# Kernel tuning notes

Hardware: AMD Instinct MI355X
Metric: run time of the kernel (lower is better)

Reference implementation:

```python
import jax, jax.numpy as jnp
import numpy as np

B, L, D, H, DFF, C = 16, 1024, 256, 4, 2048, 3
NS, NC = 4, 4
DH = D // H


def _ln(x, g, b):
    m = x.mean(-1, keepdims=True)
    v = ((x - m) ** 2).mean(-1, keepdims=True)
    return (x - m) / jnp.sqrt(v + 1e-5) * g + b


def setup_inputs() -> dict:
    key = jax.random.key(0)
    ks = jax.random.split(key, 24)
    n = lambda k, s: jax.random.normal(k, s, jnp.float32) * 0.02
    return {
        'shape_idxs': jax.random.randint(ks[0], (B, L), 0, NS, jnp.int32),
        'color_idxs': jax.random.randint(ks[1], (B, L), 0, NC, jnp.int32),
        'shape_emb': n(ks[2], (NS, D)),
        'color_emb': n(ks[3], (NC, D)),
        'Wq': n(ks[4], (D, D)), 'bq': jnp.zeros((D,)),
        'Wk': n(ks[5], (D, D)), 'bk': jnp.zeros((D,)),
        'Wv': n(ks[6], (D, D)), 'bv': jnp.zeros((D,)),
        'Wo': n(ks[7], (D, D)), 'bo': jnp.zeros((D,)),
        'g1': jnp.ones((D,)), 'be1': jnp.zeros((D,)),
        'W1': n(ks[8], (D, DFF)), 'bf1': jnp.zeros((DFF,)),
        'W2': n(ks[9], (DFF, D)), 'bf2': jnp.zeros((D,)),
        'g2': jnp.ones((D,)), 'be2': jnp.zeros((D,)),
        'Wl': n(ks[10], (D, C)), 'bl': jnp.zeros((C,)),
        'Wp1': n(ks[11], (D, D)), 'bp1': jnp.zeros((D,)),
        'Wp2': n(ks[12], (D, 1)), 'bp2': jnp.zeros((1,)),
        'wc': n(ks[13], (1, 1)), 'bc': jnp.zeros((1,)),
    }


def reference(shape_idxs, color_idxs, shape_emb, color_emb, Wq, bq, Wk, bk, Wv, bv,
              Wo, bo, g1, be1, W1, bf1, W2, bf2, g2, be2, Wl, bl,
              Wp1, bp1, Wp2, bp2, wc, bc):
    # embed (dropout is identity in eval)
    x = shape_emb[shape_idxs] + color_emb[color_idxs]  # [B,L,D]
    # post-norm transformer encoder layer (PyTorch default)
    heads = lambda t: t.reshape(B, L, H, DH)
    q, k, v = heads(x @ Wq + bq), heads(x @ Wk + bk), heads(x @ Wv + bv)
    scores = jnp.einsum('blhd,bmhd->bhlm', q, k) / jnp.sqrt(jnp.float32(DH))
    attn = jax.nn.softmax(scores, axis=-1)
    ctx = jnp.einsum('bhlm,bmhd->blhd', attn, v).reshape(B, L, D)
    y = _ln(x + ctx @ Wo + bo, g1, be1)
    ff = jax.nn.relu(y @ W1 + bf1) @ W2 + bf2
    y = _ln(y + ff, g2, be2)  # trans_out [B,L,D]
    # latent logits / KL(prior || probs) with batchmean reduction
    logits = y @ Wl + bl
    logp = jax.nn.log_softmax(logits, axis=-1)
    prior = 1.0 / C
    kl_loss = jnp.sum(prior * (jnp.log(jnp.float32(prior)) - logp)) / B
    # data-dependent boundary segmentation (argmax of probs == argmax of logits)
    boundaries = (jnp.argmax(logits, axis=-1) == 0)
    boundaries = boundaries.at[:, 0].set(True)
    closed = boundaries & (jnp.arange(L) > 0)  # closure at l>0 ends segment at l
    seg_id = jnp.cumsum(closed.astype(jnp.int32), axis=1) - closed  # exclusive cumsum
    gid = (jnp.arange(B)[:, None] * L + seg_id).reshape(-1)  # global segment ids
    sums = jax.ops.segment_sum(y.reshape(B * L, D), gid, num_segments=B * L)
    counts = jax.ops.segment_sum(jnp.ones((B * L,), jnp.float32), gid, num_segments=B * L)
    means = sums / jnp.maximum(counts, 1.0)[:, None]  # per-segment mean [B*L,D]
    # predicate net + composition, mean over valid segments
    preds = jax.nn.sigmoid(jax.nn.relu(means @ Wp1 + bp1) @ Wp2 + bp2)  # [B*L,1]
    comp = (preds * wc[0, 0] + bc[0]).reshape(B, L)
    valid = (counts > 0).reshape(B, L).astype(jnp.float32)
    mean_comp = jnp.sum(comp * valid, axis=1) / jnp.sum(valid, axis=1)
    final_scores = jax.nn.sigmoid(mean_comp)
    return final_scores, kl_loss
```

## Files before the change

### kernel.cpp

```cpp
#include <hip/hip_runtime.h>


typedef unsigned short u16;
typedef u16    u16x4  __attribute__((ext_vector_type(4)));
typedef u16    u16x8  __attribute__((ext_vector_type(8)));
typedef __bf16 bf16x8 __attribute__((ext_vector_type(8)));
typedef float  f32x4  __attribute__((ext_vector_type(4)));

__device__ __forceinline__ float bf2f(u16 u) {
    union { unsigned int i; float f; } v; v.i = ((unsigned int)u) << 16; return v.f;
}
__device__ __forceinline__ u16 f2bf(float f) {
    union { float f; unsigned int i; } v; v.f = f;
    unsigned int r = (v.i + 0x7FFFu + ((v.i >> 16) & 1u)) >> 16;
    return (u16)r;
}
__device__ __forceinline__ u16 f2bf_fast(float f) {
    union { __bf16 h; u16 u; } v; v.h = (__bf16)f; return v.u;
}
__device__ __forceinline__ void gll16(const u16* g, u16* l) {
    __builtin_amdgcn_global_load_lds((__attribute__((address_space(1))) void*)(u16*)g,
                                     (__attribute__((address_space(3))) void*)l, 16, 0, 0);
}

__global__ void k_dzero(int* __restrict__ diag, float* __restrict__ acc) {
    int t = threadIdx.x;
    if (t < 16) diag[t] = 0;
    if (t < 33) acc[t] = 0.f;
}
__global__ __launch_bounds__(256) void k_detect(const u16* __restrict__ w1raw,
                                                int* __restrict__ diag) {
    int i = blockIdx.x * 256 + threadIdx.x;
    int bad = 0;
    for (int k = i; k < 65536; k += 64 * 256) {
        unsigned v = w1raw[k] & 0x7FFFu;
        if (v >= 0x7F80u) bad++;
    }
    for (int off = 32; off >= 1; off >>= 1) bad += __shfl_xor(bad, off);
    __shared__ int bs[4];
    if ((threadIdx.x & 63) == 0) bs[threadIdx.x >> 6] = bad;
    __syncthreads();
    if (threadIdx.x == 0) {
        int tot = bs[0] + bs[1] + bs[2] + bs[3];
        if (tot) atomicAdd(&diag[14], tot);
        __threadfence();
        int ticket = atomicAdd(&diag[13], 1);
        if (ticket == 63) {
            int cnt = atomicAdd(&diag[14], 0);
            diag[15] = (cnt > 16) ? 1 : 0;
        }
    }
}

struct IngestTab {
    const void* src[26];
    unsigned    dstoff[26];
    int         n[26];
    float       scale[26];
};
__global__ __launch_bounds__(256) void k_ingest(IngestTab tab, u16* __restrict__ ing,
                                                const int* __restrict__ diag) {
    int t = blockIdx.y;
    int n = tab.n[t];
    int m = diag[15];
    float sc = tab.scale[t];
    u16* dst = ing + tab.dstoff[t];
    for (int i = blockIdx.x * 256 + threadIdx.x; i < n; i += gridDim.x * 256) {
        float v = m ? ((const float*)tab.src[t])[i] : bf2f(((const u16*)tab.src[t])[i]);
        dst[i] = f2bf(v * sc);
    }
}
__global__ void k_sentinel_f32(float* __restrict__ out, int code) {
    int t = threadIdx.x;
    if (t < 17) out[t] = (float)code;
}

struct TransTab {
    const u16* src[7];
    u16*       dst[7];
    int        K[7], N[7];
    int        tstart[8];
};
__global__ __launch_bounds__(256) void k_trans_all(TransTab tt) {
    __shared__ u16 tile[32][33];
    int bx = blockIdx.x;
    int wgt = 0;
#pragma unroll
    for (int i = 1; i < 7; ++i) if (bx >= tt.tstart[i]) wgt = i;
    int local = bx - tt.tstart[wgt];
    int K = tt.K[wgt], N = tt.N[wgt];
    int ntx = N >> 5;
    int txt = local % ntx, tyt = local / ntx;
    const u16* W = tt.src[wgt];
    u16* Wt = tt.dst[wgt];
    int tx = threadIdx.x & 31, ty = threadIdx.x >> 5;
    int n = txt * 32 + tx;
    for (int i = ty; i < 32; i += 8) {
        int k = tyt * 32 + i;
        tile[i][tx] = W[(size_t)k * N + n];
    }
    __syncthreads();
    int k2 = tyt * 32 + tx;
    for (int i = ty; i < 32; i += 8) {
        int n2 = txt * 32 + i;
        Wt[(size_t)n2 * K + k2] = tile[tx][i];
    }
}

__global__ __launch_bounds__(256) void k_embed(const int* __restrict__ si,
                                               const int* __restrict__ ci,
                                               const u16* __restrict__ se,
                                               const u16* __restrict__ ce,
                                               u16* __restrict__ X) {
    int t = blockIdx.x * 256 + threadIdx.x;
    int row = t >> 5, seg = (t & 31) * 8;
    int s = si[row], c = ci[row];
    u16x8 a = *(const u16x8*)&se[s * 256 + seg];
    u16x8 b = *(const u16x8*)&ce[c * 256 + seg];
    u16x8 o;
#pragma unroll
    for (int e = 0; e < 8; ++e) o[e] = f2bf(bf2f(a[e]) + bf2f(b[e]));
    *(u16x8*)&X[(size_t)row * 256 + seg] = o;
}

__global__ __launch_bounds__(256) void k_gemm_bt(const u16* __restrict__ A,
                                                 const u16* __restrict__ Bt,
                                                 const u16* __restrict__ bias,
                                                 u16* __restrict__ C,
                                                 int N, int K, int relu, int gx) {
    __shared__ u16 As[128][32];
    __shared__ u16 Bs[128][32];
    const int tid = threadIdx.x;
    const int xcd = blockIdx.x & 7, j = blockIdx.x >> 3;
    const int m0 = (xcd * 16 + j / gx) * 128, n0 = (j % gx) * 128;
    const int lane = tid & 63, wid = tid >> 6;
    const int wm = (wid & 1) * 64, wn = (wid >> 1) * 64;
    const int m16 = lane & 15, quad = lane >> 4;
    f32x4 acc[4][4] = {};
    const int arow = tid >> 2;
    const int ac8  = (tid & 3) * 8;
    const u16* Ap0 = A  + (size_t)(m0 + arow) * K + ac8;
    const u16* Ap1 = A  + (size_t)(m0 + 64 + arow) * K + ac8;
    const u16* Bp0 = Bt + (size_t)(n0 + arow) * K + ac8;
    const u16* Bp1 = Bt + (size_t)(n0 + 64 + arow) * K + ac8;
    u16* lA0 = &As[arow][ac8];
    u16* lA1 = &As[64 + arow][ac8];
    u16* lB0 = &Bs[arow][ac8];
    u16* lB1 = &Bs[64 + arow][ac8];

    for (int k0 = 0; k0 < K; k0 += 32) {
        __syncthreads();
        gll16(Ap0 + k0, lA0);
        gll16(Ap1 + k0, lA1);
        gll16(Bp0 + k0, lB0);
        gll16(Bp1 + k0, lB1);
        __syncthreads();
        bf16x8 af[4], bfv[4];
#pragma unroll
        for (int i = 0; i < 4; ++i)
            af[i] = *(const bf16x8*)&As[wm + i * 16 + m16][quad * 8];
#pragma unroll
        for (int j2 = 0; j2 < 4; ++j2)
            bfv[j2] = *(const bf16x8*)&Bs[wn + j2 * 16 + m16][quad * 8];
#pragma unroll
        for (int i = 0; i < 4; ++i)
#pragma unroll
            for (int j2 = 0; j2 < 4; ++j2)
                acc[i][j2] = __builtin_amdgcn_mfma_f32_16x16x32_bf16(
                    af[i], bfv[j2], acc[i][j2], 0, 0, 0);
    }

#pragma unroll
    for (int i = 0; i < 4; ++i) {
        int row = m0 + wm + i * 16 + quad * 4;
#pragma unroll
        for (int j2 = 0; j2 < 4; ++j2) {
            int col = n0 + wn + j2 * 16 + m16;
            float bv = bf2f(bias[col]);
#pragma unroll
            for (int r = 0; r < 4; ++r) {
                float v = acc[i][j2][r] + bv;
                if (relu) v = fmaxf(v, 0.f);
                C[(size_t)(row + r) * N + col] = f2bf_fast(v);
            }
        }
    }
}

__global__ __launch_bounds__(256) void k_gemm64(const u16* __restrict__ A,
                                                const u16* __restrict__ Bt,
                                                const u16* __restrict__ bias,
                                                u16* __restrict__ C,
                                                int N, int K, int relu,
                                                int gx, int mtpx,
                                                const float* __restrict__ gate,
                                                u16* __restrict__ vt) {
    __shared__ u16 As0[64][32], As1[64][32];
    __shared__ u16 Bs0[128][32], Bs1[128][32];
    const int tid = threadIdx.x;
    const int xcd = blockIdx.x & 7, j = blockIdx.x >> 3;
    const int m0 = (xcd * mtpx + j / gx) * 64, n0 = (j % gx) * 128;
    if (gate && gate[m0] == 0.f) return;
    const int vmode = (vt != nullptr) && (n0 >= 512);
    const int lane = tid & 63, wid = tid >> 6;
    const int wm = (wid & 1) * 32, wn = (wid >> 1) * 64;
    const int m16 = lane & 15, quad = lane >> 4;
    f32x4 acc[2][4] = {};
    const int arow = tid >> 2;
    const int ac8  = (tid & 3) * 8;
    const u16* Ap  = A  + (size_t)(m0 + arow) * K + ac8;
    const u16* Bp0 = Bt + (size_t)(n0 + arow) * K + ac8;
    const u16* Bp1 = Bt + (size_t)(n0 + 64 + arow) * K + ac8;
    u16* lA0  = &As0[arow][ac8];
    u16* lA1  = &As1[arow][ac8];
    u16* lB00 = &Bs0[arow][ac8];
    u16* lB01 = &Bs0[64 + arow][ac8];
    u16* lB10 = &Bs1[arow][ac8];
    u16* lB11 = &Bs1[64 + arow][ac8];

    for (int k0 = 0; k0 < K; k0 += 64) {
        __syncthreads();
        gll16(Ap + k0,        lA0);
        gll16(Ap + k0 + 32,   lA1);
        gll16(Bp0 + k0,       lB00);
        gll16(Bp0 + k0 + 32,  lB10);
        gll16(Bp1 + k0,       lB01);
        gll16(Bp1 + k0 + 32,  lB11);
        __syncthreads();
#pragma unroll
        for (int ks = 0; ks < 2; ++ks) {
            bf16x8 af[2], bfv[4];
#pragma unroll
            for (int i = 0; i < 2; ++i)
                af[i] = ks == 0 ? *(const bf16x8*)&As0[wm + i * 16 + m16][quad * 8]
                                : *(const bf16x8*)&As1[wm + i * 16 + m16][quad * 8];
#pragma unroll
            for (int j2 = 0; j2 < 4; ++j2)
                bfv[j2] = ks == 0 ? *(const bf16x8*)&Bs0[wn + j2 * 16 + m16][quad * 8]
                                  : *(const bf16x8*)&Bs1[wn + j2 * 16 + m16][quad * 8];
#pragma unroll
            for (int i = 0; i < 2; ++i)
#pragma unroll
                for (int j2 = 0; j2 < 4; ++j2)
                    acc[i][j2] = __builtin_amdgcn_mfma_f32_16x16x32_bf16(
                        af[i], bfv[j2], acc[i][j2], 0, 0, 0);
        }
    }

#pragma unroll
    for (int i = 0; i < 2; ++i) {
        int row = m0 + wm + i * 16 + quad * 4;
#pragma unroll
        for (int j2 = 0; j2 < 4; ++j2) {
            int col = n0 + wn + j2 * 16 + m16;
            float bv = bf2f(bias[col]);
            if (vmode) {
                int ch = col - 512;
                u16x4 o;
#pragma unroll
                for (int r = 0; r < 4; ++r) o[r] = f2bf_fast(acc[i][j2][r] + bv);
                size_t vb = ((size_t)((row >> 10) * 4 + (ch >> 6)) * 64 + (ch & 63)) * 1024
                          + (row & 1023);
                *(u16x4*)&vt[vb] = o;
            } else {
#pragma unroll
                for (int r = 0; r < 4; ++r) {
                    float v = acc[i][j2][r] + bv;
                    if (relu) v = fmaxf(v, 0.f);
                    C[(size_t)(row + r) * N + col] = f2bf_fast(v);
                }
            }
        }
    }
}

__global__ __launch_bounds__(256) void k_attn_mfma(const u16* __restrict__ QKV,
                                                   const u16* __restrict__ VT,
                                                   u16* __restrict__ CTX) {
    __shared__ u16 Ks[64][72];
    __shared__ u16 Vts[64][72];
    __shared__ u16 Ps[4][16][72];
    const int tid = threadIdx.x, lane = tid & 63, w = tid >> 6;
    const int quad = lane >> 4, c = lane & 15;
    const int blk = blockIdx.x;
    const int xcd = blk & 7, local = blk >> 3;
    const int bh = xcd * 8 + (local >> 4);
    const int qt = local & 15;
    const int b = bh >> 2, h = bh & 3;
    const int qrow0 = b * 1024 + qt * 64;

    const u16* qptr = QKV + (size_t)(qrow0 + w * 16 + c) * 768 + h * 64;
    bf16x8 aq0 = *(const bf16x8*)(qptr + quad * 8);
    bf16x8 aq1 = *(const bf16x8*)(qptr + 32 + quad * 8);

    f32x4 acc_o[4] = {};
    float l_part[4] = {0.f, 0.f, 0.f, 0.f};

    const u16* kbase  = QKV + (size_t)(b * 1024) * 768 + 256 + h * 64;
    const u16* vtbase = VT + (size_t)(bh * 64) * 1024;
    const int skk = tid >> 3, sc8 = (tid & 7) * 8;

    for (int t = 0; t < 16; ++t) {
        __syncthreads();
#pragma unroll
        for (int it = 0; it < 2; ++it) {
            int rr = skk + 32 * it;
            *(u16x8*)&Ks[rr][sc8]  = *(const u16x8*)(kbase + (size_t)(t * 64 + rr) * 768 + sc8);
            *(u16x8*)&Vts[rr][sc8] = *(const u16x8*)(vtbase + (size_t)rr * 1024 + t * 64 + sc8);
        }
        __syncthreads();

        f32x4 s[4];
#pragma unroll
        for (int nt = 0; nt < 4; ++nt) {
            f32x4 z = {};
            bf16x8 bk0 = *(const bf16x8*)&Ks[nt * 16 + c][quad * 8];
            bf16x8 bk1 = *(const bf16x8*)&Ks[nt * 16 + c][32 + quad * 8];
            z = __builtin_amdgcn_mfma_f32_16x16x32_bf16(aq0, bk0, z, 0, 0, 0);
            s[nt] = __builtin_amdgcn_mfma_f32_16x16x32_bf16(aq1, bk1, z, 0, 0, 0);
        }

#pragma unroll
        for (int nt = 0; nt < 4; ++nt)
#pragma unroll
            for (int r = 0; r < 4; ++r) {
                float pv = exp2f(fminf(s[nt][r], 80.f));
                l_part[r] += pv;
                Ps[w][quad * 4 + r][nt * 16 + c] = f2bf_fast(pv);
            }

#pragma unroll
        for (int ks = 0; ks < 2; ++ks) {
            bf16x8 ap = *(const bf16x8*)&Ps[w][c][ks * 32 + quad * 8];
#pragma unroll
            for (int nt = 0; nt < 4; ++nt) {
                bf16x8 bv = *(const bf16x8*)&Vts[nt * 16 + c][ks * 32 + quad * 8];
                acc_o[nt] = __builtin_amdgcn_mfma_f32_16x16x32_bf16(ap, bv, acc_o[nt], 0, 0, 0);
            }
        }
    }

#pragma unroll
    for (int r = 0; r < 4; ++r) {
#pragma unroll
        for (int off = 1; off <= 8; off <<= 1) l_part[r] += __shfl_xor(l_part[r], off);
    }
#pragma unroll
    for (int nt = 0; nt < 4; ++nt) {
        int col = h * 64 + nt * 16 + c;
#pragma unroll
        for (int r = 0; r < 4; ++r) {
            int row = qrow0 + w * 16 + quad * 4 + r;
            CTX[(size_t)row * 256 + col] = f2bf_fast(acc_o[nt][r] / l_part[r]);
        }
    }
}

__global__ __launch_bounds__(256) void k_ln(const u16* __restrict__ A,
                                            const u16* __restrict__ R,
                                            const u16* __restrict__ g,
                                            const u16* __restrict__ be,
                                            u16* __restrict__ out) {
    int w = threadIdx.x >> 6, lane = threadIdx.x & 63;
    int row = blockIdx.x * 4 + w;
    size_t base = (size_t)row * 256 + lane * 4;
    u16x4 a4 = *(const u16x4*)&A[base];
    u16x4 r4 = *(const u16x4*)&R[base];
    float v[4];
    float s = 0.f, sq = 0.f;
#pragma unroll
    for (int j = 0; j < 4; ++j) {
        v[j] = bf2f(a4[j]) + bf2f(r4[j]);
        s += v[j]; sq += v[j] * v[j];
    }
    for (int off = 32; off >= 1; off >>= 1) { s += __shfl_xor(s, off); sq += __shfl_xor(sq, off); }
    float mean = s * (1.f / 256.f);
    float var  = sq * (1.f / 256.f) - mean * mean;
    float rs   = rsqrtf(var + 1e-5f);
    u16x4 o;
#pragma unroll
    for (int j = 0; j < 4; ++j) {
        int d = lane * 4 + j;
        o[j] = f2bf((v[j] - mean) * rs * bf2f(g[d]) + bf2f(be[d]));
    }
    *(u16x4*)&out[base] = o;
}

__global__ __launch_bounds__(256) void k_logits(const u16* __restrict__ FFO,
                                                const u16* __restrict__ Y1,
                                                const u16* __restrict__ g2,
                                                const u16* __restrict__ be2,
                                                const u16* __restrict__ Wl,
                                                const u16* __restrict__ bl,
                                                u16* __restrict__ Y2,
                                                float* __restrict__ klpart,
                                                int* __restrict__ flags) {
    const int tid = threadIdx.x, lane = tid & 63, w = tid >> 6;
    float wv[4][3], gv[4], bev[4];
#pragma unroll
    for (int j = 0; j < 4; ++j) {
        int d = lane * 4 + j;
        gv[j]  = bf2f(g2[d]);
        bev[j] = bf2f(be2[d]);
#pragma unroll
        for (int c = 0; c < 3; ++c) wv[j][c] = bf2f(Wl[d * 3 + c]);
    }
    const float b0 = bf2f(bl[0]), b1 = bf2f(bl[1]), b2 = bf2f(bl[2]);
    float klsum = 0.f;
    const int row0 = blockIdx.x * 16 + w * 4;
    for (int i = 0; i < 4; ++i) {
        int row = row0 + i;
        size_t base = (size_t)row * 256 + lane * 4;
        u16x4 f4 = *(const u16x4*)&FFO[base];
        u16x4 y4 = *(const u16x4*)&Y1[base];
        float v[4];
        float s = 0.f, sq = 0.f;
#pragma unroll
        for (int j = 0; j < 4; ++j) {
            v[j] = bf2f(f4[j]) + bf2f(y4[j]);
            s += v[j]; sq += v[j] * v[j];
        }
        for (int off = 32; off >= 1; off >>= 1) { s += __shfl_xor(s, off); sq += __shfl_xor(sq, off); }
        float mean = s * (1.f / 256.f);
        float var  = sq * (1.f / 256.f) - mean * mean;
        float rs   = rsqrtf(var + 1e-5f);
        u16x4 o;
        float a0 = 0.f, a1 = 0.f, a2 = 0.f;
#pragma unroll
        for (int j = 0; j < 4; ++j) {
            float yn = (v[j] - mean) * rs * gv[j] + bev[j];
            o[j] = f2bf(yn);
            float y = bf2f(o[j]);
            a0 += y * wv[j][0]; a1 += y * wv[j][1]; a2 += y * wv[j][2];
        }
        *(u16x4*)&Y2[base] = o;
        for (int off = 32; off >= 1; off >>= 1) {
            a0 += __shfl_xor(a0, off); a1 += __shfl_xor(a1, off); a2 += __shfl_xor(a2, off);
        }
        if (lane == 0) {
            float l0 = a0 + b0, l1 = a1 + b1, l2 = a2 + b2;
            float mx = fmaxf(l0, fmaxf(l1, l2));
            float lse = mx + __logf(__expf(l0 - mx) + __expf(l1 - mx) + __expf(l2 - mx));
            klsum += lse - (l0 + l1 + l2) * (1.f / 3.f) - 1.0986122886681098f;
            int am = 0; float bv = l0;
            if (l1 > bv) { bv = l1; am = 1; }
            if (l2 > bv) { am = 2; }
            int l = row & 1023;
            flags[row] = (am == 0 && l != 0) ? 1 : 0;
        }
    }
    __shared__ float kls[4];
    if (lane == 0) kls[w] = klsum;
    __syncthreads();
    if (tid == 0) klpart[blockIdx.x] = kls[0] + kls[1] + kls[2] + kls[3];
}

__global__ void k_scan(const int* __restrict__ flags, int* __restrict__ seg) {
    __shared__ int wsum[16];
    int b = blockIdx.x, t = threadIdx.x;
    int lane = t & 63, w = t >> 6;
    int f = flags[b * 1024 + t];
    int x = f;
#pragma unroll
    for (int off = 1; off < 64; off <<= 1) {
        int v = __shfl_up(x, off);
        if (lane >= off) x += v;
    }
    if (lane == 63) wsum[w] = x;
    __syncthreads();
    if (w == 0) {
        int s = (lane < 16) ? wsum[lane] : 0;
#pragma unroll
        for (int off = 1; off < 16; off <<= 1) {
            int v = __shfl_up(s, off);
            if (lane >= off) s += v;
        }
        if (lane < 16) wsum[lane] = s;
    }
    __syncthreads();
    int prefix = (w > 0) ? wsum[w - 1] : 0;
    seg[b * 1024 + t] = prefix + x - f;
}

__global__ __launch_bounds__(64) void k_segmean(const u16* __restrict__ Y,
                                                const int* __restrict__ seg,
                                                u16* __restrict__ means,
                                                float* __restrict__ cnt) {
    int g = blockIdx.x, lane = threadIdx.x;
    int b = g >> 10, s = g & 1023;
    const int* sb = seg + b * 1024;
    int target = s + (lane & 1);
    int lo = 0, hi = 1024;
    while (lo < hi) {
        int mid = (lo + hi) >> 1;
        if (sb[mid] < target) lo = mid + 1; else hi = mid;
    }
    int start = __shfl(lo, 0);
    int end   = __shfl(lo, 1);
    int n = end - start;
    if (lane == 0) cnt[g] = (float)n;
    if (n <= 0) return;
    f32x4 acc = {};
    for (int row = start; row < end; ++row) {
        u16x4 y4 = *(const u16x4*)&Y[(size_t)(b * 1024 + row) * 256 + lane * 4];
        acc[0] += bf2f(y4[0]); acc[1] += bf2f(y4[1]);
        acc[2] += bf2f(y4[2]); acc[3] += bf2f(y4[3]);
    }
    float inv = 1.f / (float)n;
    u16x4 o;
#pragma unroll
    for (int j = 0; j < 4; ++j) o[j] = f2bf(acc[j] * inv);
    *(u16x4*)&means[(size_t)g * 256 + lane * 4] = o;
}

__global__ __launch_bounds__(256) void k_preds(const u16* __restrict__ T,
                                               const u16* __restrict__ Wp2,
                                               const u16* __restrict__ bp2,
                                               const u16* __restrict__ wc,
                                               const u16* __restrict__ bc,
                                               const float* __restrict__ cnt,
                                               float* __restrict__ num,
                                               float* __restrict__ den) {
    const int tid = threadIdx.x, lane = tid & 63, w = tid >> 6;
    float lwp[4];
#pragma unroll
    for (int j = 0; j < 4; ++j) lwp[j] = bf2f(Wp2[lane * 4 + j]);
    const float fb = bf2f(bp2[0]), fw = bf2f(wc[0]), fc = bf2f(bc[0]);
    float csum = 0.f, vsum = 0.f;
    const int g0 = blockIdx.x * 16 + w * 4;
    if (cnt[g0] != 0.f) {
        for (int i = 0; i < 4; ++i) {
            int g = g0 + i;
            u16x4 t4 = *(const u16x4*)&T[(size_t)g * 256 + lane * 4];
            float a = 0.f;
#pragma unroll
            for (int j = 0; j < 4; ++j) a += bf2f(t4[j]) * lwp[j];
            for (int off = 32; off >= 1; off >>= 1) a += __shfl_xor(a, off);
            if (lane == 0 && cnt[g] > 0.f) {
                float pred = 1.f / (1.f + __expf(-(a + fb)));
                csum += pred * fw + fc;
                vsum += 1.f;
            }
        }
    }
    __shared__ float cs[4], vs[4];
    if (lane == 0) { cs[w] = csum; vs[w] = vsum; }
    __syncthreads();
    if (tid == 0) {
        float c = cs[0] + cs[1] + cs[2] + cs[3];
        float v = vs[0] + vs[1] + vs[2] + vs[3];
        if (v > 0.f) {
            int b = (blockIdx.x * 16) >> 10;
            atomicAdd(&num[b], c);
            atomicAdd(&den[b], v);
        }
    }
}

__global__ void k_final(const float* __restrict__ num, const float* __restrict__ den,
                        const float* __restrict__ klp, const int* __restrict__ diag,
                        void* __restrict__ outv) {
    int t = threadIdx.x;
    float k = 0.f;
    for (int i = t; i < 1024; i += 64) k += klp[i];
    for (int off = 32; off >= 1; off >>= 1) k += __shfl_xor(k, off);
    float ktot = __shfl(k, 0);
    if (t > 16) return;
    int mode = diag[15];
    float val;
    if (t < 16) {
        float d = den[t], nm = num[t];
        if (!(d > 0.f)) d = 1.f;
        if (isnan(nm) || isinf(nm)) nm = 0.f;
        val = 1.f / (1.f + __expf(-nm / d));
    } else {
        val = ktot * (1.f / 16.f);
        if (isnan(val) || isinf(val)) val = 0.f;
    }
    if (mode) ((float*)outv)[t] = val;
    else      ((u16*)outv)[t]   = f2bf(val);
}

extern "C" void kernel_launch(void* const* d_in, const int* in_sizes, int n_in,
                              void* d_out, int out_size, void* d_ws, size_t ws_size,
                              hipStream_t stream) {
    const int* shape_idxs = (const int*)d_in[0];
    const int* color_idxs = (const int*)d_in[1];
    char* ws = (char*)d_ws;
    const size_t MB = 1024 * 1024;

    if (ws_size < 90 * MB) {
        int wsMB = (int)(ws_size >> 20); if (wsMB > 250) wsMB = 250;
        k_sentinel_f32<<<1, 32, 0, stream>>>((float*)d_out, 200 + wsMB);
        return;
    }

    u16*   X     = (u16*)(ws);
    u16*   QKVb  = (u16*)(ws + 8 * MB);
    u16*   VT    = (u16*)(ws + 32 * MB);
    u16*   CTX   = (u16*)(ws + 40 * MB);
    u16*   CTXP  = (u16*)(ws + 48 * MB);
    u16*   Y1    = (u16*)(ws + 64 * MB);
    u16*   Hb    = (u16*)(ws);
    u16*   FFO   = (u16*)(ws + 72 * MB);
    u16*   Y2    = (u16*)(ws);
    u16*   MEANS = (u16*)(ws + 24 * MB);
    u16*   TB    = (u16*)(ws + 32 * MB);
    int*   FLAGS = (int*)(ws + 80 * MB);
    int*   SEG   = (int*)(ws + 80 * MB + 65536);
    float* CNT   = (float*)(ws + 80 * MB + 131072);
    float* ACC   = (float*)(ws + 80 * MB + 196608);
    float* KLP   = (float*)(ws + 80 * MB + 262144);
    u16*   W3T   = (u16*)(ws + 81 * MB);
    u16*   WoT   = (u16*)(ws + 81 * MB + 786432);
    u16*   Wp1T  = (u16*)(ws + 81 * MB + 917504);
    u16*   W1T   = (u16*)(ws + 82 * MB);
    u16*   W2T   = (u16*)(ws + 83 * MB);
    int*   DIAG  = (int*)(ws + 84 * MB);
    u16*   ING   = (u16*)(ws + 85 * MB);

    static const int NS_[26] = {1024,1024,65536,256,65536,256,65536,256,65536,256,
                                256,256,524288,2048,524288,256,256,256,768,3,
                                65536,256,256,1,1,1};
    const float QSCALE = 0.125f * 1.44269504f;
    IngestTab tab;
    unsigned off = 0;
    for (int i = 0; i < 26; ++i) {
        tab.src[i] = d_in[2 + i];
        tab.n[i] = NS_[i];
        tab.scale[i] = 1.0f;
        if (i == 3) { tab.dstoff[3] = off; tab.dstoff[5] = off + 256; tab.dstoff[7] = off + 512; off += 768; }
        else if (i == 5 || i == 7) continue;
        else { tab.dstoff[i] = off; off += (unsigned)((NS_[i] + 8) & ~7); }
    }
    tab.scale[2] = QSCALE;
    tab.scale[3] = QSCALE;
    const u16* iSE  = ING + tab.dstoff[0];  const u16* iCE  = ING + tab.dstoff[1];
    const u16* iWq  = ING + tab.dstoff[2];  const u16* ib3  = ING + tab.dstoff[3];
    const u16* iWk  = ING + tab.dstoff[4];
    const u16* iWv  = ING + tab.dstoff[6];
    const u16* iWo  = ING + tab.dstoff[8];  const u16* ibo  = ING + tab.dstoff[9];
    const u16* ig1  = ING + tab.dstoff[10]; const u16* ibe1 = ING + tab.dstoff[11];
    const u16* iW1  = ING + tab.dstoff[12]; const u16* ibf1 = ING + tab.dstoff[13];
    const u16* iW2  = ING + tab.dstoff[14]; const u16* ibf2 = ING + tab.dstoff[15];
    const u16* ig2  = ING + tab.dstoff[16]; const u16* ibe2 = ING + tab.dstoff[17];
    const u16* iWl  = ING + tab.dstoff[18]; const u16* ibl  = ING + tab.dstoff[19];
    const u16* iWp1 = ING + tab.dstoff[20]; const u16* ibp1 = ING + tab.dstoff[21];
    const u16* iWp2 = ING + tab.dstoff[22]; const u16* ibp2 = ING + tab.dstoff[23];
    const u16* iwc  = ING + tab.dstoff[24]; const u16* ibc  = ING + tab.dstoff[25];

    k_dzero<<<1, 64, 0, stream>>>(DIAG, ACC);
    k_detect<<<64, 256, 0, stream>>>((const u16*)d_in[14], DIAG);
    k_ingest<<<dim3(256, 26), 256, 0, stream>>>(tab, ING, DIAG);

    TransTab tt;
    const u16* tsrc[7] = {iWq, iWk, iWv, iWo, iWp1, iW1, iW2};
    u16* tdst[7] = {W3T, W3T + 256 * 256, W3T + 512 * 256, WoT, Wp1T, W1T, W2T};
    int tK[7] = {256, 256, 256, 256, 256, 256, 2048};
    int tN[7] = {256, 256, 256, 256, 256, 2048, 256};
    int ts = 0;
    for (int i = 0; i < 7; ++i) {
        tt.src[i] = tsrc[i]; tt.dst[i] = tdst[i]; tt.K[i] = tK[i]; tt.N[i] = tN[i];
        tt.tstart[i] = ts;
        ts += (tK[i] >> 5) * (tN[i] >> 5);
    }
    tt.tstart[7] = ts;
    k_trans_all<<<ts, 256, 0, stream>>>(tt);

    k_embed<<<2048, 256, 0, stream>>>(shape_idxs, color_idxs, iSE, iCE, X);
    k_gemm64<<<1536, 256, 0, stream>>>(X, W3T, ib3, QKVb, 768, 256, 0, 6, 32, nullptr, VT);
    k_attn_mfma<<<1024, 256, 0, stream>>>(QKVb, VT, CTX);
    k_gemm64<<<512, 256, 0, stream>>>(CTX, WoT, ibo, CTXP, 256, 256, 0, 2, 32, nullptr, nullptr);
    k_ln<<<4096, 256, 0, stream>>>(CTXP, X, ig1, ibe1, Y1);
    k_gemm_bt<<<16 * 128, 256, 0, stream>>>(Y1, W1T, ibf1, Hb, 2048, 256, 1, 16);
    k_gemm64<<<512, 256, 0, stream>>>(Hb, W2T, ibf2, FFO, 256, 2048, 0, 2, 32, nullptr, nullptr);
    k_logits<<<1024, 256, 0, stream>>>(FFO, Y1, ig2, ibe2, iWl, ibl, Y2, KLP, FLAGS);
    k_scan<<<16, 1024, 0, stream>>>(FLAGS, SEG);
    k_segmean<<<16384, 64, 0, stream>>>(Y2, SEG, MEANS, CNT);
    k_gemm64<<<512, 256, 0, stream>>>(MEANS, Wp1T, ibp1, TB, 256, 256, 1, 2, 32, CNT, nullptr);
    k_preds<<<1024, 256, 0, stream>>>(TB, iWp2, ibp2, iwc, ibc, CNT, ACC + 1, ACC + 17);
    k_final<<<1, 64, 0, stream>>>(ACC + 1, ACC + 17, KLP, DIAG, d_out);
}
```

Measured before the change: 321.4 us.

## Fold weight ingest into transpose/embed, drop zeroing kernel, use MFMA for softmax denominators

```diff
diff --git a/kernel.cpp b/kernel.cpp
--- a/kernel.cpp
+++ b/kernel.cpp
@@ -22,14 +22,15 @@
     __builtin_amdgcn_global_load_lds((__attribute__((address_space(1))) void*)(u16*)g,
                                      (__attribute__((address_space(3))) void*)l, 16, 0, 0);
 }
-
-__global__ void k_dzero(int* __restrict__ diag, float* __restrict__ acc) {
-    int t = threadIdx.x;
-    if (t < 16) diag[t] = 0;
-    if (t < 33) acc[t] = 0.f;
-}
+__device__ __forceinline__ int get_mode(const int* __restrict__ detp) {
+    int s = 0;
+#pragma unroll 8
+    for (int i = 0; i < 64; ++i) s += detp[i];
+    return s > 16;
+}
+
 __global__ __launch_bounds__(256) void k_detect(const u16* __restrict__ w1raw,
-                                                int* __restrict__ diag) {
+                                                int* __restrict__ detp) {
     int i = blockIdx.x * 256 + threadIdx.x;
     int bad = 0;
     for (int k = i; k < 65536; k += 64 * 256) {
@@ -40,29 +41,20 @@
     __shared__ int bs[4];
     if ((threadIdx.x & 63) == 0) bs[threadIdx.x >> 6] = bad;
     __syncthreads();
-    if (threadIdx.x == 0) {
-        int tot = bs[0] + bs[1] + bs[2] + bs[3];
-        if (tot) atomicAdd(&diag[14], tot);
-        __threadfence();
-        int ticket = atomicAdd(&diag[13], 1);
-        if (ticket == 63) {
-            int cnt = atomicAdd(&diag[14], 0);
-            diag[15] = (cnt > 16) ? 1 : 0;
-        }
-    }
+    if (threadIdx.x == 0) detp[blockIdx.x] = bs[0] + bs[1] + bs[2] + bs[3];
 }
 
 struct IngestTab {
-    const void* src[26];
-    unsigned    dstoff[26];
-    int         n[26];
-    float       scale[26];
+    const void* src[17];
+    unsigned    dstoff[17];
+    int         n[17];
+    float       scale[17];
 };
 __global__ __launch_bounds__(256) void k_ingest(IngestTab tab, u16* __restrict__ ing,
-                                                const int* __restrict__ diag) {
+                                                const int* __restrict__ detp) {
     int t = blockIdx.y;
     int n = tab.n[t];
-    int m = diag[15];
+    int m = get_mode(detp);
     float sc = tab.scale[t];
     u16* dst = ing + tab.dstoff[t];
     for (int i = blockIdx.x * 256 + threadIdx.x; i < n; i += gridDim.x * 256) {
@@ -76,28 +68,33 @@
 }
 
 struct TransTab {
-    const u16* src[7];
-    u16*       dst[7];
-    int        K[7], N[7];
-    int        tstart[8];
+    const void* src[7];
+    u16*        dst[7];
+    int         K[7], N[7];
+    float       scale[7];
+    int         tstart[8];
 };
-__global__ __launch_bounds__(256) void k_trans_all(TransTab tt) {
+__global__ __launch_bounds__(256) void k_trans_all(TransTab tt,
+                                                   const int* __restrict__ detp) {
     __shared__ u16 tile[32][33];
+    int m = get_mode(detp);
     int bx = blockIdx.x;
     int wgt = 0;
 #pragma unroll
     for (int i = 1; i < 7; ++i) if (bx >= tt.tstart[i]) wgt = i;
     int local = bx - tt.tstart[wgt];
     int K = tt.K[wgt], N = tt.N[wgt];
+    float sc = tt.scale[wgt];
     int ntx = N >> 5;
     int txt = local % ntx, tyt = local / ntx;
-    const u16* W = tt.src[wgt];
+    const void* W = tt.src[wgt];
     u16* Wt = tt.dst[wgt];
     int tx = threadIdx.x & 31, ty = threadIdx.x >> 5;
     int n = txt * 32 + tx;
     for (int i = ty; i < 32; i += 8) {
-        int k = tyt * 32 + i;
-        tile[i][tx] = W[(size_t)k * N + n];
+        size_t idx = (size_t)(tyt * 32 + i) * N + n;
+        float v = m ? ((const float*)W)[idx] : bf2f(((const u16*)W)[idx]);
+        tile[i][tx] = f2bf(v * sc);
     }
     __syncthreads();
     int k2 = tyt * 32 + tx;
@@ -109,17 +106,26 @@
 
 __global__ __launch_bounds__(256) void k_embed(const int* __restrict__ si,
                                                const int* __restrict__ ci,
-                                               const u16* __restrict__ se,
-                                               const u16* __restrict__ ce,
-                                               u16* __restrict__ X) {
+                                               const void* __restrict__ se,
+                                               const void* __restrict__ ce,
+                                               u16* __restrict__ X,
+                                               const int* __restrict__ detp) {
+    int m = get_mode(detp);
     int t = blockIdx.x * 256 + threadIdx.x;
     int row = t >> 5, seg = (t & 31) * 8;
     int s = si[row], c = ci[row];
-    u16x8 a = *(const u16x8*)&se[s * 256 + seg];
-    u16x8 b = *(const u16x8*)&ce[c * 256 + seg];
     u16x8 o;
-#pragma unroll
-    for (int e = 0; e < 8; ++e) o[e] = f2bf(bf2f(a[e]) + bf2f(b[e]));
+    if (m) {
+        const float* sp = (const float*)se + s * 256 + seg;
+        const float* cp = (const float*)ce + c * 256 + seg;
+#pragma unroll
+        for (int e = 0; e < 8; ++e) o[e] = f2bf(sp[e] + cp[e]);
+    } else {
+        u16x8 a = *(const u16x8*)((const u16*)se + s * 256 + seg);
+        u16x8 b = *(const u16x8*)((const u16*)ce + c * 256 + seg);
+#pragma unroll
+        for (int e = 0; e < 8; ++e) o[e] = f2bf(bf2f(a[e]) + bf2f(b[e]));
+    }
     *(u16x8*)&X[(size_t)row * 256 + seg] = o;
 }
 
@@ -293,8 +299,15 @@
     bf16x8 aq0 = *(const bf16x8*)(qptr + quad * 8);
     bf16x8 aq1 = *(const bf16x8*)(qptr + 32 + quad * 8);
 
+    bf16x8 ones;
+    {
+        union { u16 u; __bf16 h; } v; v.u = 0x3F80;
+#pragma unroll
+        for (int e = 0; e < 8; ++e) ones[e] = v.h;
+    }
+
     f32x4 acc_o[4] = {};
-    float l_part[4] = {0.f, 0.f, 0.f, 0.f};
+    f32x4 acc_l = {};
 
     const u16* kbase  = QKV + (size_t)(b * 1024) * 768 + 256 + h * 64;
     const u16* vtbase = VT + (size_t)(bh * 64) * 1024;
@@ -323,15 +336,13 @@
 #pragma unroll
         for (int nt = 0; nt < 4; ++nt)
 #pragma unroll
-            for (int r = 0; r < 4; ++r) {
-                float pv = exp2f(fminf(s[nt][r], 80.f));
-                l_part[r] += pv;
-                Ps[w][quad * 4 + r][nt * 16 + c] = f2bf_fast(pv);
-            }
+            for (int r = 0; r < 4; ++r)
+                Ps[w][quad * 4 + r][nt * 16 + c] = f2bf_fast(exp2f(fminf(s[nt][r], 80.f)));
 
 #pragma unroll
         for (int ks = 0; ks < 2; ++ks) {
             bf16x8 ap = *(const bf16x8*)&Ps[w][c][ks * 32 + quad * 8];
+            acc_l = __builtin_amdgcn_mfma_f32_16x16x32_bf16(ap, ones, acc_l, 0, 0, 0);
 #pragma unroll
             for (int nt = 0; nt < 4; ++nt) {
                 bf16x8 bv = *(const bf16x8*)&Vts[nt * 16 + c][ks * 32 + quad * 8];
@@ -341,17 +352,12 @@
     }
 
 #pragma unroll
-    for (int r = 0; r < 4; ++r) {
-#pragma unroll
-        for (int off = 1; off <= 8; off <<= 1) l_part[r] += __shfl_xor(l_part[r], off);
-    }
-#pragma unroll
     for (int nt = 0; nt < 4; ++nt) {
         int col = h * 64 + nt * 16 + c;
 #pragma unroll
         for (int r = 0; r < 4; ++r) {
             int row = qrow0 + w * 16 + quad * 4 + r;
-            CTX[(size_t)row * 256 + col] = f2bf_fast(acc_o[nt][r] / l_part[r]);
+            CTX[(size_t)row * 256 + col] = f2bf_fast(acc_o[nt][r] / acc_l[r]);
         }
     }
 }
@@ -519,8 +525,7 @@
                                                const u16* __restrict__ wc,
                                                const u16* __restrict__ bc,
                                                const float* __restrict__ cnt,
-                                               float* __restrict__ num,
-                                               float* __restrict__ den) {
+                                               float* __restrict__ predp) {
     const int tid = threadIdx.x, lane = tid & 63, w = tid >> 6;
     float lwp[4];
 #pragma unroll
@@ -547,38 +552,42 @@
     if (lane == 0) { cs[w] = csum; vs[w] = vsum; }
     __syncthreads();
     if (tid == 0) {
-        float c = cs[0] + cs[1] + cs[2] + cs[3];
-        float v = vs[0] + vs[1] + vs[2] + vs[3];
-        if (v > 0.f) {
-            int b = (blockIdx.x * 16) >> 10;
-            atomicAdd(&num[b], c);
-            atomicAdd(&den[b], v);
-        }
-    }
-}
-
-__global__ void k_final(const float* __restrict__ num, const float* __restrict__ den,
-                        const float* __restrict__ klp, const int* __restrict__ diag,
-                        void* __restrict__ outv) {
+        predp[2 * blockIdx.x]     = cs[0] + cs[1] + cs[2] + cs[3];
+        predp[2 * blockIdx.x + 1] = vs[0] + vs[1] + vs[2] + vs[3];
+    }
+}
+
+__global__ void k_final(const float* __restrict__ predp, const float* __restrict__ klp,
+                        const int* __restrict__ detp, void* __restrict__ outv) {
     int t = threadIdx.x;
     float k = 0.f;
     for (int i = t; i < 1024; i += 64) k += klp[i];
     for (int off = 32; off >= 1; off >>= 1) k += __shfl_xor(k, off);
     float ktot = __shfl(k, 0);
-    if (t > 16) return;
-    int mode = diag[15];
-    float val;
-    if (t < 16) {
-        float d = den[t], nm = num[t];
+    int batch = t >> 2, ch = t & 3;
+    float c = 0.f, v = 0.f;
+    for (int i = 0; i < 16; ++i) {
+        int blk = batch * 64 + ch * 16 + i;
+        c += predp[2 * blk];
+        v += predp[2 * blk + 1];
+    }
+    c += __shfl_xor(c, 1); c += __shfl_xor(c, 2);
+    v += __shfl_xor(v, 1); v += __shfl_xor(v, 2);
+    int mode = get_mode(detp);
+    if ((t & 3) == 0) {
+        float d = v, nm = c;
         if (!(d > 0.f)) d = 1.f;
         if (isnan(nm) || isinf(nm)) nm = 0.f;
-        val = 1.f / (1.f + __expf(-nm / d));
-    } else {
-        val = ktot * (1.f / 16.f);
+        float val = 1.f / (1.f + __expf(-nm / d));
+        if (mode) ((float*)outv)[batch] = val;
+        else      ((u16*)outv)[batch]   = f2bf(val);
+    }
+    if (t == 1) {
+        float val = ktot * (1.f / 16.f);
         if (isnan(val) || isinf(val)) val = 0.f;
-    }
-    if (mode) ((float*)outv)[t] = val;
-    else      ((u16*)outv)[t]   = f2bf(val);
+        if (mode) ((float*)outv)[16] = val;
+        else      ((u16*)outv)[16]   = f2bf(val);
+    }
 }
 
 extern "C" void kernel_launch(void* const* d_in, const int* in_sizes, int n_in,
@@ -609,65 +618,61 @@
     int*   FLAGS = (int*)(ws + 80 * MB);
     int*   SEG   = (int*)(ws + 80 * MB + 65536);
     float* CNT   = (float*)(ws + 80 * MB + 131072);
-    float* ACC   = (float*)(ws + 80 * MB + 196608);
     float* KLP   = (float*)(ws + 80 * MB + 262144);
+    float* PREDP = (float*)(ws + 80 * MB + 327680);
     u16*   W3T   = (u16*)(ws + 81 * MB);
     u16*   WoT   = (u16*)(ws + 81 * MB + 786432);
     u16*   Wp1T  = (u16*)(ws + 81 * MB + 917504);
     u16*   W1T   = (u16*)(ws + 82 * MB);
     u16*   W2T   = (u16*)(ws + 83 * MB);
-    int*   DIAG  = (int*)(ws + 84 * MB);
+    int*   DETP  = (int*)(ws + 84 * MB);
     u16*   ING   = (u16*)(ws + 85 * MB);
 
-    static const int NS_[26] = {1024,1024,65536,256,65536,256,65536,256,65536,256,
-                                256,256,524288,2048,524288,256,256,256,768,3,
-                                65536,256,256,1,1,1};
     const float QSCALE = 0.125f * 1.44269504f;
+
+    static const int II[17]  = {5, 7, 9, 11, 12, 13, 15, 17, 18, 19, 20, 21, 23, 24, 25, 26, 27};
+    static const int IN[17]  = {256, 256, 256, 256, 256, 256, 2048, 256, 256, 256, 768, 3, 256, 256, 1, 1, 1};
     IngestTab tab;
     unsigned off = 0;
-    for (int i = 0; i < 26; ++i) {
-        tab.src[i] = d_in[2 + i];
-        tab.n[i] = NS_[i];
+    for (int i = 0; i < 17; ++i) {
+        tab.src[i] = d_in[II[i]];
+        tab.n[i] = IN[i];
         tab.scale[i] = 1.0f;
-        if (i == 3) { tab.dstoff[3] = off; tab.dstoff[5] = off + 256; tab.dstoff[7] = off + 512; off += 768; }
-        else if (i == 5 || i == 7) continue;
-        else { tab.dstoff[i] = off; off += (unsigned)((NS_[i] + 8) & ~7); }
-    }
-    tab.scale[2] = QSCALE;
-    tab.scale[3] = QSCALE;
-    const u16* iSE  = ING + tab.dstoff[0];  const u16* iCE  = ING + tab.dstoff[1];
-    const u16* iWq  = ING + tab.dstoff[2];  const u16* ib3  = ING + tab.dstoff[3];
-    const u16* iWk  = ING + tab.dstoff[4];
-    const u16* iWv  = ING + tab.dstoff[6];
-    const u16* iWo  = ING + tab.dstoff[8];  const u16* ibo  = ING + tab.dstoff[9];
-    const u16* ig1  = ING + tab.dstoff[10]; const u16* ibe1 = ING + tab.dstoff[11];
-    const u16* iW1  = ING + tab.dstoff[12]; const u16* ibf1 = ING + tab.dstoff[13];
-    const u16* iW2  = ING + tab.dstoff[14]; const u16* ibf2 = ING + tab.dstoff[15];
-    const u16* ig2  = ING + tab.dstoff[16]; const u16* ibe2 = ING + tab.dstoff[17];
-    const u16* iWl  = ING + tab.dstoff[18]; const u16* ibl  = ING + tab.dstoff[19];
-    const u16* iWp1 = ING + tab.dstoff[20]; const u16* ibp1 = ING + tab.dstoff[21];
-    const u16* iWp2 = ING + tab.dstoff[22]; const u16* ibp2 = ING + tab.dstoff[23];
-    const u16* iwc  = ING + tab.dstoff[24]; const u16* ibc  = ING + tab.dstoff[25];
-
-    k_dzero<<<1, 64, 0, stream>>>(DIAG, ACC);
-    k_detect<<<64, 256, 0, stream>>>((const u16*)d_in[14], DIAG);
-    k_ingest<<<dim3(256, 26), 256, 0, stream>>>(tab, ING, DIAG);
+        if (i == 0) { tab.dstoff[0] = off; off += 768; }
+        else if (i == 1) tab.dstoff[1] = tab.dstoff[0] + 256;
+        else if (i == 2) tab.dstoff[2] = tab.dstoff[0] + 512;
+        else { tab.dstoff[i] = off; off += (unsigned)((IN[i] + 8) & ~7); }
+    }
+    tab.scale[0] = QSCALE;
+    const u16* ib3  = ING + tab.dstoff[0];
+    const u16* ibo  = ING + tab.dstoff[3];
+    const u16* ig1  = ING + tab.dstoff[4];  const u16* ibe1 = ING + tab.dstoff[5];
+    const u16* ibf1 = ING + tab.dstoff[6];  const u16* ibf2 = ING + tab.dstoff[7];
+    const u16* ig2  = ING + tab.dstoff[8];  const u16* ibe2 = ING + tab.dstoff[9];
+    const u16* iWl  = ING + tab.dstoff[10]; const u16* ibl  = ING + tab.dstoff[11];
+    const u16* ibp1 = ING + tab.dstoff[12]; const u16* iWp2 = ING + tab.dstoff[13];
+    const u16* ibp2 = ING + tab.dstoff[14]; const u16* iwc  = ING + tab.dstoff[15];
+    const u16* ibc  = ING + tab.dstoff[16];
+
+    k_detect<<<64, 256, 0, stream>>>((const u16*)d_in[14], DETP);
+    k_ingest<<<dim3(8, 17), 256, 0, stream>>>(tab, ING, DETP);
 
     TransTab tt;
-    const u16* tsrc[7] = {iWq, iWk, iWv, iWo, iWp1, iW1, iW2};
+    const void* tsrc[7] = {d_in[4], d_in[6], d_in[8], d_in[10], d_in[22], d_in[14], d_in[16]};
     u16* tdst[7] = {W3T, W3T + 256 * 256, W3T + 512 * 256, WoT, Wp1T, W1T, W2T};
     int tK[7] = {256, 256, 256, 256, 256, 256, 2048};
     int tN[7] = {256, 256, 256, 256, 256, 2048, 256};
     int ts = 0;
     for (int i = 0; i < 7; ++i) {
         tt.src[i] = tsrc[i]; tt.dst[i] = tdst[i]; tt.K[i] = tK[i]; tt.N[i] = tN[i];
+        tt.scale[i] = (i == 0) ? QSCALE : 1.0f;
         tt.tstart[i] = ts;
         ts += (tK[i] >> 5) * (tN[i] >> 5);
     }
     tt.tstart[7] = ts;
-    k_trans_all<<<ts, 256, 0, stream>>>(tt);
-
-    k_embed<<<2048, 256, 0, stream>>>(shape_idxs, color_idxs, iSE, iCE, X);
+    k_trans_all<<<ts, 256, 0, stream>>>(tt, DETP);
+
+    k_embed<<<2048, 256, 0, stream>>>(shape_idxs, color_idxs, d_in[2], d_in[3], X, DETP);
     k_gemm64<<<1536, 256, 0, stream>>>(X, W3T, ib3, QKVb, 768, 256, 0, 6, 32, nullptr, VT);
     k_attn_mfma<<<1024, 256, 0, stream>>>(QKVb, VT, CTX);
     k_gemm64<<<512, 256, 0, stream>>>(CTX, WoT, ibo, CTXP, 256, 256, 0, 2, 32, nullptr, nullptr);
@@ -678,6 +683,6 @@
     k_scan<<<16, 1024, 0, stream>>>(FLAGS, SEG);
     k_segmean<<<16384, 64, 0, stream>>>(Y2, SEG, MEANS, CNT);
     k_gemm64<<<512, 256, 0, stream>>>(MEANS, Wp1T, ibp1, TB, 256, 256, 1, 2, 32, CNT, nullptr);
-    k_preds<<<1024, 256, 0, stream>>>(TB, iWp2, ibp2, iwc, ibc, CNT, ACC + 1, ACC + 17);
-    k_final<<<1, 64, 0, stream>>>(ACC + 1, ACC + 17, KLP, DIAG, d_out);
-}
+    k_preds<<<1024, 256, 0, stream>>>(TB, iWp2, ibp2, iwc, ibc, CNT, PREDP);
+    k_final<<<1, 64, 0, stream>>>(PREDP, KLP, DETP, d_out);
+}
```

Result: faster. 308.1 us (-4.1%).
